# Kernel optimization log

Hardware: AMD Instinct MI355X
Metric: run time of the kernel (lower is better)

## Reference

```python
import jax, jax.numpy as jnp
import numpy as np

NUM_HEADS = 16

def setup_inputs() -> dict:
    key = jax.random.key(0)
    ks = jax.random.split(key, 6)
    B, N, E = 2, 2048, 2048
    QK, V, M = 2048, 2048, 4096
    x = jax.random.normal(ks[0], (B, N, E), dtype=jnp.float32)
    Wq = jax.random.normal(ks[1], (QK, E), dtype=jnp.float32) * 0.02
    k_weight = jax.random.normal(ks[2], (M, QK), dtype=jnp.float32) * 0.05
    v_weight = jax.random.normal(ks[3], (M, V), dtype=jnp.float32) * 0.05
    Wg = jax.random.normal(ks[4], (V, E), dtype=jnp.float32) * 0.02
    Wout = jax.random.normal(ks[5], (E, V), dtype=jnp.float32) * 0.02
    return {"x": x, "Wq": Wq, "k_weight": k_weight, "v_weight": v_weight, "Wg": Wg, "Wout": Wout}

def reference(x, Wq, k_weight, v_weight, Wg, Wout):
    H = NUM_HEADS
    B, N, E = x.shape
    M = k_weight.shape[0]
    # q: [B, N, QK] -> [B, H, N, dk]
    q = jnp.einsum('bne,fe->bnf', x, Wq)
    dk = q.shape[-1] // H
    q = q.reshape(B, N, H, dk).transpose(0, 2, 1, 3)
    # k: [M, QK] -> [H, M, dk]; v: [M, V] -> [H, M, dv]
    k = k_weight.reshape(M, H, dk).transpose(1, 0, 2)
    dv = v_weight.shape[1] // H
    v = v_weight.reshape(M, H, dv).transpose(1, 0, 2)
    scale = jnp.asarray(dk, x.dtype) ** 0.5  # use_scale == 1
    k = k * scale
    v = v * scale
    # non-softmax attention over fixed memory
    energy = jax.nn.silu(jnp.einsum('bhnd,hmd->bhnm', q, k))  # [B,H,N,M]
    out = jnp.einsum('bhnm,hmd->bhnd', energy, v)  # [B,H,N,dv]
    out = out.transpose(0, 2, 1, 3).reshape(B, N, H * dv)
    # output gate (silu)
    gate = jax.nn.silu(jnp.einsum('bne,ve->bnv', x, Wg))
    out = out * gate
    return jnp.einsum('bnv,ev->bne', out, Wout)
```

## Files before the change

### kernel.cpp

```cpp
#include <hip/hip_runtime.h>

typedef __bf16 bf16;
typedef __bf16 bf16x4 __attribute__((ext_vector_type(4)));
typedef __bf16 bf16x8 __attribute__((ext_vector_type(8)));
typedef float f32x4 __attribute__((ext_vector_type(4)));

#define MFMA(a, b, c) __builtin_amdgcn_mfma_f32_16x16x32_bf16(a, b, c, 0, 0, 0)

__device__ __forceinline__ float fast_silu(float x) {
  float e = __builtin_amdgcn_exp2f(x * -1.4426950408889634f);
  return x * __builtin_amdgcn_rcpf(1.f + e);
}

__device__ __forceinline__ void gload_lds16(const void* g, void* l) {
  __builtin_amdgcn_global_load_lds(
      (const __attribute__((address_space(1))) void*)g,
      (__attribute__((address_space(3))) void*)l, 16, 0, 0);
}

__global__ __launch_bounds__(256) void cvt_bf16(const float* __restrict__ in,
                                                bf16* __restrict__ out, int n) {
  int i = (blockIdx.x * 256 + threadIdx.x) * 4;
  if (i >= n) return;
  float4 v = *(const float4*)(in + i);
  bf16x4 o = {(bf16)v.x, (bf16)v.y, (bf16)v.z, (bf16)v.w};
  *(bf16x4*)(out + i) = o;
}

__global__ __launch_bounds__(256) void transpose_v_cvt(const float* __restrict__ v,
                                                       bf16* __restrict__ vt) {
  __shared__ bf16 T[64 * 72];
  const int m0 = blockIdx.x * 64, c0 = blockIdx.y * 64;
  const int tid = threadIdx.x;
  const int tr = tid >> 3;
  const int tc = (tid & 7) << 3;
#pragma unroll
  for (int it = 0; it < 2; it++) {
    int r = tr + it * 32;
    const float* src = v + (long)(m0 + r) * 2048 + c0 + tc;
    float4 a = *(const float4*)src;
    float4 b = *(const float4*)(src + 4);
    bf16x8 t = {(bf16)a.x, (bf16)a.y, (bf16)a.z, (bf16)a.w,
                (bf16)b.x, (bf16)b.y, (bf16)b.z, (bf16)b.w};
    *(bf16x8*)&T[r * 72 + tc] = t;
  }
  __syncthreads();
#pragma unroll
  for (int it = 0; it < 2; it++) {
    int c = tr + it * 32;
    bf16x8 o;
#pragma unroll
    for (int j = 0; j < 8; j++) o[j] = T[(tc + j) * 72 + c];
    *(bf16x8*)(vt + (long)(c0 + c) * 4096 + m0 + tc) = o;
  }
}

template <int MODE>
__global__ __launch_bounds__(256, 2) void gemm_bt(const bf16* __restrict__ A,
                                                  const bf16* __restrict__ B,
                                                  const bf16* __restrict__ B2,
                                                  bf16* __restrict__ C1,
                                                  bf16* __restrict__ C2,
                                                  float* __restrict__ Cf, int M, int N, int K) {
  __shared__ bf16 As[128 * 32];
  __shared__ bf16 Bs[128 * 32];
  const int tid = threadIdx.x;
  const int wave = tid >> 6, lane = tid & 63;
  const int wr = wave >> 1, wc = wave & 1;
  const bool gsel = (MODE == 3) && (blockIdx.x >= 16);
  const bf16* Bm = gsel ? B2 : B;
  const long bM = (long)blockIdx.y * 128;
  const long bN = (long)((MODE == 3) ? (blockIdx.x & 15) : blockIdx.x) * 128;

  f32x4 acc[4][4] = {};

  const int srow = (wave << 5) + (lane >> 2);
  const int sg = ((lane & 3) ^ ((lane >> 3) & 3)) << 3;
  const bf16* Ag = A + (bM + srow) * (long)K + sg;
  const bf16* Bg = Bm + (bN + srow) * (long)K + sg;
  bf16* Asl = &As[srow * 32 + ((lane & 3) << 3)];
  bf16* Bsl = &Bs[srow * 32 + ((lane & 3) << 3)];

  const int fr = lane & 15;
  const int gofs = (((lane >> 4) ^ ((fr >> 1) & 3)) << 3);

  for (int k0 = 0; k0 < K; k0 += 32) {
    __syncthreads();
    gload_lds16(Ag + k0, Asl);
    gload_lds16(Ag + k0 + (long)16 * K, Asl + 16 * 32);
    gload_lds16(Bg + k0, Bsl);
    gload_lds16(Bg + k0 + (long)16 * K, Bsl + 16 * 32);
    __syncthreads();
    bf16x8 af[4], bfv[4];
#pragma unroll
    for (int i = 0; i < 4; i++)
      af[i] = *(const bf16x8*)&As[(wr * 64 + i * 16 + fr) * 32 + gofs];
#pragma unroll
    for (int j = 0; j < 4; j++)
      bfv[j] = *(const bf16x8*)&Bs[(wc * 64 + j * 16 + fr) * 32 + gofs];
#pragma unroll
    for (int i = 0; i < 4; i++)
#pragma unroll
      for (int j = 0; j < 4; j++) acc[i][j] = MFMA(af[i], bfv[j], acc[i][j]);
  }

  const int er = wr * 64 + ((lane >> 4) << 2);
  const int ec = wc * 64 + (lane & 15);
#pragma unroll
  for (int i = 0; i < 4; i++)
#pragma unroll
    for (int j = 0; j < 4; j++)
#pragma unroll
      for (int r = 0; r < 4; r++) {
        long row = bM + er + i * 16 + r;
        long col = bN + ec + j * 16;
        float v = acc[i][j][r];
        if (MODE == 2) {
          Cf[row * (long)N + col] = v;
        } else {
          if (gsel)
            C2[row * (long)N + col] = (bf16)fast_silu(v);
          else
            C1[row * (long)N + col] = (bf16)(v * 11.3137085f);
        }
      }
}

__global__ __launch_bounds__(512, 4) void attn_fused(const bf16* __restrict__ q,
                                                     const bf16* __restrict__ kw,
                                                     const bf16* __restrict__ vt,
                                                     bf16* __restrict__ gate_io) {
  constexpr int E = 2048, M = 4096;
  constexpr float scale = 11.3137085f;
  const int bid = blockIdx.x;
  const int h = ((bid & 7) << 1) | ((bid >> 8) & 1);
  const int sub = (bid >> 3) & 31;
  const int b = sub >> 4, nt = sub & 15;
  const long n0 = (long)b * 2048 + nt * 128;

  const int tid = threadIdx.x, wave = tid >> 6, lane = tid & 63;
  const int quad = lane >> 4, ln = lane & 15;
  const int sw_m = wave & 1, sw_n = wave >> 1;
  const int pw_n = wave & 3, pw_dv = wave >> 2;

  __shared__ bf16 Ks[2][64 * 128];
  __shared__ bf16 Vts[2][128 * 64];
  __shared__ bf16 Ps[128 * 64];

  const bf16* qbase = q + (n0 + sw_n * 32) * E + h * 128;
  bf16x8 qf[2][4];
#pragma unroll
  for (int n2 = 0; n2 < 2; n2++)
#pragma unroll
    for (int ks = 0; ks < 4; ks++)
      qf[n2][ks] = *(const bf16x8*)(qbase + (long)(n2 * 16 + ln) * E + ks * 32 + (quad << 3));

  f32x4 oacc[2][4] = {};

  const bf16* kg = kw + (long)((wave << 3) + quad) * E + h * 128;
  const int ksl_off = (wave << 3) * 128 + lane * 8;
  int kc[2];
#pragma unroll
  for (int i = 0; i < 2; i++) kc[i] = (ln ^ ((wave * 8 + i * 4 + quad) & 15)) << 3;

  const bf16* vg = vt + (long)(h * 128 + (wave << 4) + (lane >> 3)) * M +
                   (((lane & 7) ^ ((lane >> 3) & 7)) << 3);
  const int vsl_off = (wave << 4) * 64 + lane * 8;

  int waddr[2][2];
#pragma unroll
  for (int mt = 0; mt < 2; mt++)
#pragma unroll
    for (int n2 = 0; n2 < 2; n2++) {
      int n = sw_n * 32 + n2 * 16 + ln;
      int mb8 = sw_m * 4 + mt * 2 + (quad >> 1);
      waddr[mt][n2] = n * 64 + ((mb8 ^ (n & 7)) << 3) + ((quad & 1) << 2);
    }

  auto stage = [&](int ms, int sb) {
#pragma unroll
    for (int i = 0; i < 2; i++) {
      gload_lds16(kg + (long)(ms + i * 4) * E + kc[i], &Ks[sb][ksl_off + i * 4 * 128]);
      gload_lds16(vg + ms + (long)i * 8 * M, &Vts[sb][vsl_off + i * 8 * 64]);
    }
  };

  stage(0, 0);
  asm volatile("s_waitcnt vmcnt(0)" ::: "memory");
  __builtin_amdgcn_s_barrier();

  auto body = [&](int m0, int rb, int sb, bool doStage) {
    if (doStage) stage(m0 + 64, sb);

    f32x4 sacc[2][2] = {};
    __builtin_amdgcn_s_setprio(1);
#pragma unroll
    for (int ks = 0; ks < 4; ks++) {
      bf16x8 af[2];
#pragma unroll
      for (int mt = 0; mt < 2; mt++)
        af[mt] = *(const bf16x8*)&Ks[rb][(sw_m * 32 + mt * 16 + ln) * 128 +
                                         (((ks * 4 + quad) ^ ln) << 3)];
#pragma unroll
      for (int mt = 0; mt < 2; mt++)
#pragma unroll
        for (int n2 = 0; n2 < 2; n2++) sacc[mt][n2] = MFMA(af[mt], qf[n2][ks], sacc[mt][n2]);
    }
    __builtin_amdgcn_s_setprio(0);

#pragma unroll
    for (int mt = 0; mt < 2; mt++)
#pragma unroll
      for (int n2 = 0; n2 < 2; n2++) {
        bf16x4 p;
#pragma unroll
        for (int r = 0; r < 4; r++) p[r] = (bf16)fast_silu(sacc[mt][n2][r]);
        *(bf16x4*)&Ps[waddr[mt][n2]] = p;
      }

    asm volatile("s_waitcnt lgkmcnt(0)" ::: "memory");
    __builtin_amdgcn_s_barrier();

#pragma unroll
    for (int ks = 0; ks < 2; ks++) {
      const int so = ((ks * 4 + quad) ^ (ln & 7)) << 3;
      bf16x8 pf[2], vf[4];
#pragma unroll
      for (int n2 = 0; n2 < 2; n2++)
        pf[n2] = *(const bf16x8*)&Ps[(pw_n * 32 + n2 * 16 + ln) * 64 + so];
#pragma unroll
      for (int dt = 0; dt < 4; dt++)
        vf[dt] = *(const bf16x8*)&Vts[rb][(pw_dv * 64 + dt * 16 + ln) * 64 + so];
      __builtin_amdgcn_s_setprio(1);
#pragma unroll
      for (int n2 = 0; n2 < 2; n2++)
#pragma unroll
        for (int dt = 0; dt < 4; dt++) oacc[n2][dt] = MFMA(pf[n2], vf[dt], oacc[n2][dt]);
      __builtin_amdgcn_s_setprio(0);
    }

    asm volatile("s_waitcnt vmcnt(0)" ::: "memory");
    __builtin_amdgcn_s_barrier();
  };

  for (int m0 = 0; m0 < M; m0 += 128) {
    body(m0, 0, 1, true);
    body(m0 + 64, 1, 0, m0 + 128 < M);
  }

  bf16* gio = gate_io + n0 * E + h * 128;
#pragma unroll
  for (int n2 = 0; n2 < 2; n2++)
#pragma unroll
    for (int dt = 0; dt < 4; dt++)
#pragma unroll
      for (int r = 0; r < 4; r++) {
        int n = pw_n * 32 + n2 * 16 + quad * 4 + r;
        int dv = pw_dv * 64 + dt * 16 + ln;
        float g = (float)gio[(long)n * E + dv];
        gio[(long)n * E + dv] = (bf16)(g * oacc[n2][dt][r] * scale);
      }
}

extern "C" void kernel_launch(void* const* d_in, const int* in_sizes, int n_in,
                              void* d_out, int out_size, void* d_ws, size_t ws_size,
                              hipStream_t stream) {
  const float* x = (const float*)d_in[0];
  const float* Wq = (const float*)d_in[1];
  const float* kw = (const float*)d_in[2];
  const float* vw = (const float*)d_in[3];
  const float* Wg = (const float*)d_in[4];
  const float* Wout = (const float*)d_in[5];
  float* out = (float*)d_out;
  bf16* ws = (bf16*)d_ws;

  bf16* S0 = ws;
  bf16* S1 = ws + 8388608;
  bf16* S2 = ws + 16777216;
  bf16* S3 = ws + 25165824;
  bf16* S4 = ws + 33554432;
  bf16* Wgb = S1 + 4194304;

  cvt_bf16<<<8192, 256, 0, stream>>>(x, S0, 8388608);
  cvt_bf16<<<4096, 256, 0, stream>>>(Wq, S1, 4194304);
  cvt_bf16<<<4096, 256, 0, stream>>>(Wg, Wgb, 4194304);
  transpose_v_cvt<<<dim3(64, 32), 256, 0, stream>>>(vw, S2);
  gemm_bt<3><<<dim3(32, 32), 256, 0, stream>>>(S0, S1, Wgb, S3, S4, (float*)nullptr, 4096, 2048,
                                               2048);
  cvt_bf16<<<8192, 256, 0, stream>>>(kw, S0, 8388608);
  attn_fused<<<512, 512, 0, stream>>>(S3, S0, S2, S4);
  cvt_bf16<<<4096, 256, 0, stream>>>(Wout, S1, 4194304);
  gemm_bt<2><<<dim3(16, 32), 256, 0, stream>>>(S4, S1, (const bf16*)nullptr, (bf16*)nullptr,
                                               (bf16*)nullptr, out, 4096, 2048, 2048);
}
```

Baseline: 470.9 us.

## Enlarge attention tile to 256 rows with software-pipelined single-barrier loop

The fused attention kernel now runs 1024-thread blocks that each cover 256 query rows instead of 128. This halves the grid and the number of times each head's K/V memory tiles are streamed from global memory. The main loop becomes a skewed software pipeline: the score GEMM for tile t overlaps the P·V GEMM for tile t-1, using double-buffered P and V staging, with a single __syncthreads per iteration instead of two barriers. In exchange, LDS use per block grows and there is only one block per CU. The kernel also relies on __syncthreads to wait for the async global-to-LDS loads.

```diff
diff --git a/kernel.cpp b/kernel.cpp
--- a/kernel.cpp
+++ b/kernel.cpp
@@ -126,26 +126,26 @@
       }
 }
 
-__global__ __launch_bounds__(512, 4) void attn_fused(const bf16* __restrict__ q,
-                                                     const bf16* __restrict__ kw,
-                                                     const bf16* __restrict__ vt,
-                                                     bf16* __restrict__ gate_io) {
+__global__ __launch_bounds__(1024, 4) void attn_fused(const bf16* __restrict__ q,
+                                                      const bf16* __restrict__ kw,
+                                                      const bf16* __restrict__ vt,
+                                                      bf16* __restrict__ gate_io) {
   constexpr int E = 2048, M = 4096;
   constexpr float scale = 11.3137085f;
   const int bid = blockIdx.x;
-  const int h = ((bid & 7) << 1) | ((bid >> 8) & 1);
-  const int sub = (bid >> 3) & 31;
-  const int b = sub >> 4, nt = sub & 15;
-  const long n0 = (long)b * 2048 + nt * 128;
+  const int xcd = bid & 7, sub = bid >> 3;
+  const int h = (xcd << 1) | (sub >> 4);
+  const int b = (sub >> 3) & 1, nt = sub & 7;
+  const long n0 = (long)b * 2048 + nt * 256;
 
   const int tid = threadIdx.x, wave = tid >> 6, lane = tid & 63;
   const int quad = lane >> 4, ln = lane & 15;
   const int sw_m = wave & 1, sw_n = wave >> 1;
-  const int pw_n = wave & 3, pw_dv = wave >> 2;
+  const int pw_n = wave & 7, pw_dv = wave >> 3;
 
   __shared__ bf16 Ks[2][64 * 128];
   __shared__ bf16 Vts[2][128 * 64];
-  __shared__ bf16 Ps[128 * 64];
+  __shared__ bf16 Ps[2][256 * 64];
 
   const bf16* qbase = q + (n0 + sw_n * 32) * E + h * 128;
   bf16x8 qf[2][4];
@@ -157,15 +157,13 @@
 
   f32x4 oacc[2][4] = {};
 
-  const bf16* kg = kw + (long)((wave << 3) + quad) * E + h * 128;
-  const int ksl_off = (wave << 3) * 128 + lane * 8;
-  int kc[2];
-#pragma unroll
-  for (int i = 0; i < 2; i++) kc[i] = (ln ^ ((wave * 8 + i * 4 + quad) & 15)) << 3;
-
-  const bf16* vg = vt + (long)(h * 128 + (wave << 4) + (lane >> 3)) * M +
+  const bf16* kg = kw + (long)((wave << 2) + quad) * E + h * 128 +
+                   ((ln ^ ((wave * 4 + quad) & 15)) << 3);
+  const int kdst = (wave << 2) * 128 + lane * 8;
+
+  const bf16* vg = vt + (long)(h * 128 + (wave << 3) + (lane >> 3)) * M +
                    (((lane & 7) ^ ((lane >> 3) & 7)) << 3);
-  const int vsl_off = (wave << 4) * 64 + lane * 8;
+  const int vdst = (wave << 3) * 64 + lane * 8;
 
   int waddr[2][2];
 #pragma unroll
@@ -177,75 +175,65 @@
       waddr[mt][n2] = n * 64 + ((mb8 ^ (n & 7)) << 3) + ((quad & 1) << 2);
     }
 
-  auto stage = [&](int ms, int sb) {
-#pragma unroll
-    for (int i = 0; i < 2; i++) {
-      gload_lds16(kg + (long)(ms + i * 4) * E + kc[i], &Ks[sb][ksl_off + i * 4 * 128]);
-      gload_lds16(vg + ms + (long)i * 8 * M, &Vts[sb][vsl_off + i * 8 * 64]);
-    }
-  };
-
-  stage(0, 0);
+  gload_lds16(kg, &Ks[0][kdst]);
   asm volatile("s_waitcnt vmcnt(0)" ::: "memory");
   __builtin_amdgcn_s_barrier();
 
-  auto body = [&](int m0, int rb, int sb, bool doStage) {
-    if (doStage) stage(m0 + 64, sb);
+  for (int t = 0; t <= 64; ++t) {
+    const int cur = t & 1, prv = cur ^ 1;
+    if (t < 63) gload_lds16(kg + (long)(t + 1) * 64 * E, &Ks[prv][kdst]);
+    if (t < 64) gload_lds16(vg + t * 64, &Vts[cur][vdst]);
 
     f32x4 sacc[2][2] = {};
-    __builtin_amdgcn_s_setprio(1);
-#pragma unroll
-    for (int ks = 0; ks < 4; ks++) {
-      bf16x8 af[2];
+    if (t < 64) {
+      __builtin_amdgcn_s_setprio(1);
+#pragma unroll
+      for (int ks = 0; ks < 4; ks++) {
+        bf16x8 af[2];
+#pragma unroll
+        for (int mt = 0; mt < 2; mt++)
+          af[mt] = *(const bf16x8*)&Ks[cur][(sw_m * 32 + mt * 16 + ln) * 128 +
+                                           (((ks * 4 + quad) ^ ln) << 3)];
+#pragma unroll
+        for (int mt = 0; mt < 2; mt++)
+#pragma unroll
+          for (int n2 = 0; n2 < 2; n2++) sacc[mt][n2] = MFMA(af[mt], qf[n2][ks], sacc[mt][n2]);
+      }
+      __builtin_amdgcn_s_setprio(0);
+    }
+
+    if (t > 0) {
+#pragma unroll
+      for (int ks = 0; ks < 2; ks++) {
+        const int so = ((ks * 4 + quad) ^ (ln & 7)) << 3;
+        bf16x8 pf[2], vf[4];
+#pragma unroll
+        for (int n2 = 0; n2 < 2; n2++)
+          pf[n2] = *(const bf16x8*)&Ps[prv][(pw_n * 32 + n2 * 16 + ln) * 64 + so];
+#pragma unroll
+        for (int dt = 0; dt < 4; dt++)
+          vf[dt] = *(const bf16x8*)&Vts[prv][(pw_dv * 64 + dt * 16 + ln) * 64 + so];
+        __builtin_amdgcn_s_setprio(1);
+#pragma unroll
+        for (int n2 = 0; n2 < 2; n2++)
+#pragma unroll
+          for (int dt = 0; dt < 4; dt++) oacc[n2][dt] = MFMA(pf[n2], vf[dt], oacc[n2][dt]);
+        __builtin_amdgcn_s_setprio(0);
+      }
+    }
+
+    if (t < 64) {
 #pragma unroll
       for (int mt = 0; mt < 2; mt++)
-        af[mt] = *(const bf16x8*)&Ks[rb][(sw_m * 32 + mt * 16 + ln) * 128 +
-                                         (((ks * 4 + quad) ^ ln) << 3)];
-#pragma unroll
-      for (int mt = 0; mt < 2; mt++)
-#pragma unroll
-        for (int n2 = 0; n2 < 2; n2++) sacc[mt][n2] = MFMA(af[mt], qf[n2][ks], sacc[mt][n2]);
-    }
-    __builtin_amdgcn_s_setprio(0);
-
-#pragma unroll
-    for (int mt = 0; mt < 2; mt++)
-#pragma unroll
-      for (int n2 = 0; n2 < 2; n2++) {
-        bf16x4 p;
-#pragma unroll
-        for (int r = 0; r < 4; r++) p[r] = (bf16)fast_silu(sacc[mt][n2][r]);
-        *(bf16x4*)&Ps[waddr[mt][n2]] = p;
-      }
-
-    asm volatile("s_waitcnt lgkmcnt(0)" ::: "memory");
-    __builtin_amdgcn_s_barrier();
-
-#pragma unroll
-    for (int ks = 0; ks < 2; ks++) {
-      const int so = ((ks * 4 + quad) ^ (ln & 7)) << 3;
-      bf16x8 pf[2], vf[4];
-#pragma unroll
-      for (int n2 = 0; n2 < 2; n2++)
-        pf[n2] = *(const bf16x8*)&Ps[(pw_n * 32 + n2 * 16 + ln) * 64 + so];
-#pragma unroll
-      for (int dt = 0; dt < 4; dt++)
-        vf[dt] = *(const bf16x8*)&Vts[rb][(pw_dv * 64 + dt * 16 + ln) * 64 + so];
-      __builtin_amdgcn_s_setprio(1);
-#pragma unroll
-      for (int n2 = 0; n2 < 2; n2++)
-#pragma unroll
-        for (int dt = 0; dt < 4; dt++) oacc[n2][dt] = MFMA(pf[n2], vf[dt], oacc[n2][dt]);
-      __builtin_amdgcn_s_setprio(0);
-    }
-
-    asm volatile("s_waitcnt vmcnt(0)" ::: "memory");
-    __builtin_amdgcn_s_barrier();
-  };
-
-  for (int m0 = 0; m0 < M; m0 += 128) {
-    body(m0, 0, 1, true);
-    body(m0 + 64, 1, 0, m0 + 128 < M);
+#pragma unroll
+        for (int n2 = 0; n2 < 2; n2++) {
+          bf16x4 p;
+#pragma unroll
+          for (int r = 0; r < 4; r++) p[r] = (bf16)fast_silu(sacc[mt][n2][r]);
+          *(bf16x4*)&Ps[cur][waddr[mt][n2]] = p;
+        }
+      __syncthreads();
+    }
   }
 
   bf16* gio = gate_io + n0 * E + h * 128;
@@ -288,7 +276,7 @@
   gemm_bt<3><<<dim3(32, 32), 256, 0, stream>>>(S0, S1, Wgb, S3, S4, (float*)nullptr, 4096, 2048,
                                                2048);
   cvt_bf16<<<8192, 256, 0, stream>>>(kw, S0, 8388608);
-  attn_fused<<<512, 512, 0, stream>>>(S3, S0, S2, S4);
+  attn_fused<<<256, 1024, 0, stream>>>(S3, S0, S2, S4);
   cvt_bf16<<<4096, 256, 0, stream>>>(Wout, S1, 4194304);
   gemm_bt<2><<<dim3(16, 32), 256, 0, stream>>>(S4, S1, (const bf16*)nullptr, (bf16*)nullptr,
                                                (bf16*)nullptr, out, 4096, 2048, 2048);
```

After: 464.8 us. No clear change (-1.3%).

## Replace 128x128 GEMM with double-buffered 256-wide tiled GEMM with staged prefetch

Applied to the files above, without the earlier changes.

Replaces the 128x128, K=32, single-buffered projection GEMM with a 512-thread kernel that uses 256x256 or 128x256 tiles, K=64 steps and double-buffered LDS. Loads for the next K tile are split into four chunks and interleaved with four MFMA phases, using s_setprio around the MFMA phases. Block IDs are remapped so neighbouring blocks share input panels. The aim is more data reuse per LDS load and hiding global-load latency behind MFMA work, at the cost of more registers and LDS, fewer blocks, and many more barriers.

```diff
diff --git a/kernel.cpp b/kernel.cpp
--- a/kernel.cpp
+++ b/kernel.cpp
@@ -55,66 +55,150 @@
   }
 }
 
-template <int MODE>
-__global__ __launch_bounds__(256, 2) void gemm_bt(const bf16* __restrict__ A,
+template <int MODE, int BM>
+__global__ __launch_bounds__(512, 2) void gemm256(const bf16* __restrict__ A,
                                                   const bf16* __restrict__ B,
                                                   const bf16* __restrict__ B2,
                                                   bf16* __restrict__ C1,
                                                   bf16* __restrict__ C2,
-                                                  float* __restrict__ Cf, int M, int N, int K) {
-  __shared__ bf16 As[128 * 32];
-  __shared__ bf16 Bs[128 * 32];
-  const int tid = threadIdx.x;
-  const int wave = tid >> 6, lane = tid & 63;
-  const int wr = wave >> 1, wc = wave & 1;
-  const bool gsel = (MODE == 3) && (blockIdx.x >= 16);
+                                                  float* __restrict__ Cf, int K, int N) {
+  constexpr int MR = BM / 32;
+  constexpr int MR2 = MR / 2;
+  constexpr int NA = BM / 64;
+  __shared__ bf16 As[2][BM * 64];
+  __shared__ bf16 Bs[2][256 * 64];
+
+  const int tid = threadIdx.x, wave = tid >> 6, lane = tid & 63;
+  const int wr = wave >> 2, wc = wave & 3;
+  const int quad = lane >> 4, fr = lane & 15;
+
+  const int id2 = (blockIdx.x & 7) * 32 + (blockIdx.x >> 3);
+  const int gx = (MODE == 3) ? (id2 >> 4) : (id2 >> 5);
+  const int gy = (MODE == 3) ? (id2 & 15) : (id2 & 31);
+  const bool gsel = (MODE == 3) && (gx >= 8);
   const bf16* Bm = gsel ? B2 : B;
-  const long bM = (long)blockIdx.y * 128;
-  const long bN = (long)((MODE == 3) ? (blockIdx.x & 15) : blockIdx.x) * 128;
-
-  f32x4 acc[4][4] = {};
-
-  const int srow = (wave << 5) + (lane >> 2);
-  const int sg = ((lane & 3) ^ ((lane >> 3) & 3)) << 3;
-  const bf16* Ag = A + (bM + srow) * (long)K + sg;
-  const bf16* Bg = Bm + (bN + srow) * (long)K + sg;
-  bf16* Asl = &As[srow * 32 + ((lane & 3) << 3)];
-  bf16* Bsl = &Bs[srow * 32 + ((lane & 3) << 3)];
-
-  const int fr = lane & 15;
-  const int gofs = (((lane >> 4) ^ ((fr >> 1) & 3)) << 3);
-
-  for (int k0 = 0; k0 < K; k0 += 32) {
+  const long bM = (long)gy * BM;
+  const long bN = (long)((MODE == 3) ? (gx & 7) : gx) * 256;
+
+  f32x4 acc[MR][4] = {};
+
+  const int srow = tid >> 3;
+  const int sblk = (tid & 7) ^ (srow & 7);
+  const bf16* Ag = A + (bM + srow) * (long)K + (sblk << 3);
+  const bf16* Bg = Bm + (bN + srow) * (long)K + (sblk << 3);
+  const int sdst = srow * 64 + ((tid & 7) << 3);
+
+  auto stA = [&](int kt, int sb, int i) {
+    gload_lds16(Ag + (long)i * 64 * K + kt * 64, &As[sb][sdst + i * 64 * 64]);
+  };
+  auto stB = [&](int kt, int sb, int i) {
+    gload_lds16(Bg + (long)i * 64 * K + kt * 64, &Bs[sb][sdst + i * 64 * 64]);
+  };
+  auto rdA = [&](int rb, int mi, int kk) {
+    int row = wr * (BM / 2) + mi * 16 + fr;
+    return *(const bf16x8*)&As[rb][row * 64 + (((kk * 4 + quad) ^ (fr & 7)) << 3)];
+  };
+  auto rdB = [&](int rb, int ni, int kk) {
+    int row = wc * 64 + ni * 16 + fr;
+    return *(const bf16x8*)&Bs[rb][row * 64 + (((kk * 4 + quad) ^ (fr & 7)) << 3)];
+  };
+
+#pragma unroll
+  for (int i = 0; i < NA; i++) stA(0, 0, i);
+#pragma unroll
+  for (int i = 0; i < 4; i++) stB(0, 0, i);
+  __syncthreads();
+
+  const int NT = K >> 6;
+  for (int kt = 0; kt < NT; ++kt) {
+    const int rb = kt & 1, sb = rb ^ 1;
+    const bool st = (kt + 1) < NT;
+    bf16x8 bfv[4][2], ah[MR2][2];
+
+#pragma unroll
+    for (int ni = 0; ni < 4; ni++)
+#pragma unroll
+      for (int kk = 0; kk < 2; kk++) bfv[ni][kk] = rdB(rb, ni, kk);
+#pragma unroll
+    for (int mi = 0; mi < MR2; mi++)
+#pragma unroll
+      for (int kk = 0; kk < 2; kk++) ah[mi][kk] = rdA(rb, mi, kk);
+    if (st) {
+      if (BM == 256) { stA(kt + 1, sb, 0); stA(kt + 1, sb, 1); }
+      else { stA(kt + 1, sb, 0); stB(kt + 1, sb, 0); }
+    }
+    __builtin_amdgcn_s_barrier();
+    __builtin_amdgcn_s_setprio(1);
+#pragma unroll
+    for (int mi = 0; mi < MR2; mi++)
+#pragma unroll
+      for (int ni = 0; ni < 2; ni++)
+#pragma unroll
+        for (int kk = 0; kk < 2; kk++) acc[mi][ni] = MFMA(ah[mi][kk], bfv[ni][kk], acc[mi][ni]);
+    __builtin_amdgcn_s_setprio(0);
+    __builtin_amdgcn_s_barrier();
+
+    if (st) {
+      if (BM == 256) { stA(kt + 1, sb, 2); stA(kt + 1, sb, 3); }
+      else { stA(kt + 1, sb, 1); stB(kt + 1, sb, 1); }
+    }
+    __builtin_amdgcn_s_barrier();
+    __builtin_amdgcn_s_setprio(1);
+#pragma unroll
+    for (int mi = 0; mi < MR2; mi++)
+#pragma unroll
+      for (int ni = 2; ni < 4; ni++)
+#pragma unroll
+        for (int kk = 0; kk < 2; kk++) acc[mi][ni] = MFMA(ah[mi][kk], bfv[ni][kk], acc[mi][ni]);
+    __builtin_amdgcn_s_setprio(0);
+    __builtin_amdgcn_s_barrier();
+
+#pragma unroll
+    for (int mi = 0; mi < MR2; mi++)
+#pragma unroll
+      for (int kk = 0; kk < 2; kk++) ah[mi][kk] = rdA(rb, mi + MR2, kk);
+    if (st) {
+      if (BM == 256) { stB(kt + 1, sb, 0); stB(kt + 1, sb, 1); }
+      else { stB(kt + 1, sb, 2); }
+    }
+    __builtin_amdgcn_s_barrier();
+    __builtin_amdgcn_s_setprio(1);
+#pragma unroll
+    for (int mi = 0; mi < MR2; mi++)
+#pragma unroll
+      for (int ni = 0; ni < 2; ni++)
+#pragma unroll
+        for (int kk = 0; kk < 2; kk++)
+          acc[mi + MR2][ni] = MFMA(ah[mi][kk], bfv[ni][kk], acc[mi + MR2][ni]);
+    __builtin_amdgcn_s_setprio(0);
+    __builtin_amdgcn_s_barrier();
+
+    if (st) {
+      if (BM == 256) { stB(kt + 1, sb, 2); stB(kt + 1, sb, 3); }
+      else { stB(kt + 1, sb, 3); }
+    }
+    __builtin_amdgcn_s_barrier();
+    __builtin_amdgcn_s_setprio(1);
+#pragma unroll
+    for (int mi = 0; mi < MR2; mi++)
+#pragma unroll
+      for (int ni = 2; ni < 4; ni++)
+#pragma unroll
+        for (int kk = 0; kk < 2; kk++)
+          acc[mi + MR2][ni] = MFMA(ah[mi][kk], bfv[ni][kk], acc[mi + MR2][ni]);
+    __builtin_amdgcn_s_setprio(0);
     __syncthreads();
-    gload_lds16(Ag + k0, Asl);
-    gload_lds16(Ag + k0 + (long)16 * K, Asl + 16 * 32);
-    gload_lds16(Bg + k0, Bsl);
-    gload_lds16(Bg + k0 + (long)16 * K, Bsl + 16 * 32);
-    __syncthreads();
-    bf16x8 af[4], bfv[4];
-#pragma unroll
-    for (int i = 0; i < 4; i++)
-      af[i] = *(const bf16x8*)&As[(wr * 64 + i * 16 + fr) * 32 + gofs];
-#pragma unroll
-    for (int j = 0; j < 4; j++)
-      bfv[j] = *(const bf16x8*)&Bs[(wc * 64 + j * 16 + fr) * 32 + gofs];
-#pragma unroll
-    for (int i = 0; i < 4; i++)
-#pragma unroll
-      for (int j = 0; j < 4; j++) acc[i][j] = MFMA(af[i], bfv[j], acc[i][j]);
   }
 
-  const int er = wr * 64 + ((lane >> 4) << 2);
-  const int ec = wc * 64 + (lane & 15);
-#pragma unroll
-  for (int i = 0; i < 4; i++)
-#pragma unroll
-    for (int j = 0; j < 4; j++)
+#pragma unroll
+  for (int mi = 0; mi < MR; mi++)
+#pragma unroll
+    for (int ni = 0; ni < 4; ni++)
 #pragma unroll
       for (int r = 0; r < 4; r++) {
-        long row = bM + er + i * 16 + r;
-        long col = bN + ec + j * 16;
-        float v = acc[i][j][r];
+        long row = bM + wr * (BM / 2) + mi * 16 + quad * 4 + r;
+        long col = bN + wc * 64 + ni * 16 + fr;
+        float v = acc[mi][ni][r];
         if (MODE == 2) {
           Cf[row * (long)N + col] = v;
         } else {
@@ -285,11 +369,10 @@
   cvt_bf16<<<4096, 256, 0, stream>>>(Wq, S1, 4194304);
   cvt_bf16<<<4096, 256, 0, stream>>>(Wg, Wgb, 4194304);
   transpose_v_cvt<<<dim3(64, 32), 256, 0, stream>>>(vw, S2);
-  gemm_bt<3><<<dim3(32, 32), 256, 0, stream>>>(S0, S1, Wgb, S3, S4, (float*)nullptr, 4096, 2048,
-                                               2048);
+  gemm256<3, 256><<<256, 512, 0, stream>>>(S0, S1, Wgb, S3, S4, (float*)nullptr, 2048, 2048);
   cvt_bf16<<<8192, 256, 0, stream>>>(kw, S0, 8388608);
   attn_fused<<<512, 512, 0, stream>>>(S3, S0, S2, S4);
   cvt_bf16<<<4096, 256, 0, stream>>>(Wout, S1, 4194304);
-  gemm_bt<2><<<dim3(16, 32), 256, 0, stream>>>(S4, S1, (const bf16*)nullptr, (bf16*)nullptr,
-                                               (bf16*)nullptr, out, 4096, 2048, 2048);
-}
+  gemm256<2, 128><<<256, 512, 0, stream>>>(S4, S1, (const bf16*)nullptr, (bf16*)nullptr,
+                                           (bf16*)nullptr, out, 2048, 2048);
+}
```

Result: faster. 460.3 us (-2.3%).
